# Performance work log

Hardware: AMD Instinct MI355X
Metric: run time of the kernel (lower is better)

## Reference

```python
import jax, jax.numpy as jnp
import numpy as np

N = 50000      # graph nodes
E = 400000     # random edges (plus N self-loops)
F = 128        # graph feature dim
H = 4          # GAT heads (layer1)
DH = 64        # gnn_hidden_size (per-head out, layer1)
EMB = 8        # emb_size / GAT final out
B = 16384      # batch
NS = 20        # number of sparse features
V = 1000       # vocab per sparse feature
DENSE = 64     # num_fea_size
HID = 256      # hidden_dims
EPS = 1e-5


def setup_inputs():
    key = jax.random.key(0)
    ks = jax.random.split(key, 40)
    loop = jnp.arange(N, dtype=jnp.int32)
    src = jnp.concatenate([jax.random.randint(ks[0], (E,), 0, N, dtype=jnp.int32), loop])
    dst = jnp.concatenate([jax.random.randint(ks[1], (E,), 0, N, dtype=jnp.int32), loop])
    s = 0.05
    d = {
        'X_id': jax.random.randint(ks[2], (B, 2), 0, N),
        'X_sparse': jax.random.randint(ks[3], (B, NS), 0, V),
        'X_dense': jax.random.normal(ks[4], (B, DENSE), jnp.float32),
        'emb_tables': jax.random.normal(ks[5], (NS, V, EMB), jnp.float32) * s,
        'graph_feature': jax.random.normal(ks[6], (N, F), jnp.float32),
        'src': src, 'dst': dst,
        'wide_w': jax.random.normal(ks[7], (EMB, DENSE), jnp.float32) * s,
        'wide_b': jnp.zeros((EMB,), jnp.float32),
        'lin1_w': jax.random.normal(ks[8], (HID, NS * EMB + DENSE), jnp.float32) * s,
        'lin1_b': jnp.zeros((HID,), jnp.float32),
        'bn1_g': jnp.ones((HID,), jnp.float32),
        'bn1_b': jnp.zeros((HID,), jnp.float32),
        'bn1_m': jax.random.normal(ks[9], (HID,), jnp.float32) * s,
        'bn1_v': jnp.ones((HID,), jnp.float32),
        'lin2_w': jax.random.normal(ks[10], (HID, HID), jnp.float32) * s,
        'lin2_b': jnp.zeros((HID,), jnp.float32),
        'bn2_g': jnp.ones((HID,), jnp.float32),
        'bn2_b': jnp.zeros((HID,), jnp.float32),
        'bn2_m': jax.random.normal(ks[11], (HID,), jnp.float32) * s,
        'bn2_v': jnp.ones((HID,), jnp.float32),
        'dnn_w': jax.random.normal(ks[12], (EMB, HID), jnp.float32) * s,
        'dnn_b': jnp.zeros((EMB,), jnp.float32),
        'gat1_w': jax.random.normal(ks[13], (H * DH, F), jnp.float32) * s,
        'gat1_al': jax.random.normal(ks[14], (H, DH), jnp.float32) * s,
        'gat1_ar': jax.random.normal(ks[15], (H, DH), jnp.float32) * s,
        'gat1_bias': jnp.zeros((H * DH,), jnp.float32),
        'gat2_w': jax.random.normal(ks[16], (EMB, H * DH), jnp.float32) * s,
        'gat2_al': jax.random.normal(ks[17], (1, EMB), jnp.float32) * s,
        'gat2_ar': jax.random.normal(ks[18], (1, EMB), jnp.float32) * s,
        'gat2_bias': jnp.zeros((EMB,), jnp.float32),
        'g1w': jax.random.normal(ks[19], (1, EMB), jnp.float32) * s,
        'g1b': jnp.zeros((1,), jnp.float32),
        'g2w': jax.random.normal(ks[20], (1, EMB), jnp.float32) * s,
        'g2b': jnp.zeros((1,), jnp.float32),
        'g3w': jax.random.normal(ks[21], (1, EMB), jnp.float32) * s,
        'g3b': jnp.zeros((1,), jnp.float32),
        'gout_w': jax.random.normal(ks[22], (2, 3 * EMB), jnp.float32) * s,
        'gout_b': jnp.zeros((2,), jnp.float32),
    }
    return d


def gat_conv(h, W, al, ar, bias, src, dst, heads, dh):
    # DGL GATConv: project, per-edge attention, edge-softmax over dst, aggregate
    feat = (h @ W.T).reshape(-1, heads, dh)          # [N, H, D]
    el = (feat * al).sum(-1)                          # [N, H] src score
    er = (feat * ar).sum(-1)                          # [N, H] dst score
    e = jax.nn.leaky_relu(el[src] + er[dst], 0.2)     # [Etot, H]
    emax = jax.lax.stop_gradient(jax.ops.segment_max(e, dst, num_segments=N))
    a = jnp.exp(e - emax[dst])
    denom = jax.ops.segment_sum(a, dst, num_segments=N)  # [N, H]
    alpha = a / denom[dst]                            # [Etot, H]
    out = jax.ops.segment_sum(alpha[:, :, None] * feat[src], dst, num_segments=N)
    return out + bias.reshape(1, heads, dh)           # [N, H, D]


def batchnorm_eval(x, g, b, m, v):
    return g * (x - m) * jax.lax.rsqrt(v + EPS) + b


def reference(X_id, X_sparse, X_dense, emb_tables, graph_feature, src, dst,
              wide_w, wide_b, lin1_w, lin1_b, bn1_g, bn1_b, bn1_m, bn1_v,
              lin2_w, lin2_b, bn2_g, bn2_b, bn2_m, bn2_v, dnn_w, dnn_b,
              gat1_w, gat1_al, gat1_ar, gat1_bias, gat2_w, gat2_al, gat2_ar, gat2_bias,
              g1w, g1b, g2w, g2b, g3w, g3b, gout_w, gout_b):
    commit_ids = X_id[:, 1]
    # sparse embedding lookup: [B, NS, EMB] -> [B, NS*EMB]
    sparse_embed = emb_tables[jnp.arange(NS)[None, :], X_sparse].reshape(B, NS * EMB)
    x = jnp.concatenate([sparse_embed, X_dense], axis=-1)
    wide_out = X_dense @ wide_w.T + wide_b            # [B, EMB]
    # deep MLP (eval-mode BN, dropout = identity)
    d = jax.nn.relu(batchnorm_eval(x @ lin1_w.T + lin1_b, bn1_g, bn1_b, bn1_m, bn1_v))
    d = jax.nn.relu(batchnorm_eval(d @ lin2_w.T + lin2_b, bn2_g, bn2_b, bn2_m, bn2_v))
    deep_out = d @ dnn_w.T + dnn_b                    # [B, EMB]
    # GAT
    h1 = gat_conv(graph_feature, gat1_w, gat1_al, gat1_ar, gat1_bias, src, dst, H, DH)
    h1 = jax.nn.elu(h1.reshape(N, H * DH))
    h2 = gat_conv(h1, gat2_w, gat2_al, gat2_ar, gat2_bias, src, dst, 1, EMB)
    gcn = h2.reshape(N, EMB)                          # squeeze head dim
    gcn_out = gcn[commit_ids]                         # [B, EMB]
    # Gate (concat)
    aw = jax.nn.sigmoid(wide_out @ g1w.T + g1b)
    bw = jax.nn.sigmoid(deep_out @ g2w.T + g2b)
    cw = jax.nn.sigmoid(gcn_out @ g3w.T + g3b)
    tot = aw + bw + cw
    combined = jnp.concatenate([(aw / tot) * wide_out, (bw / tot) * deep_out,
                                (cw / tot) * gcn_out], axis=1)
    out = combined @ gout_w.T + gout_b                # [B, 2]
    return jax.nn.softmax(out, axis=1)
```

## Files before the change

kernel.cpp:

```cpp
#include <hip/hip_runtime.h>

#define TPB 256
#define DCAP 64
constexpr float BN_EPS = 1e-5f;

typedef __attribute__((ext_vector_type(8))) short short8;
typedef __attribute__((ext_vector_type(4))) float floatx4;

__device__ __forceinline__ float sigmoidf_(float x) { return 1.f / (1.f + __expf(-x)); }
__device__ __forceinline__ unsigned short f2bf(float f) {
    unsigned u = __float_as_uint(f);
    u += 0x7FFFu + ((u >> 16) & 1u);
    return (unsigned short)(u >> 16);
}
__device__ __forceinline__ float bf2f(unsigned short h) {
    return __uint_as_float((unsigned)h << 16);
}

__global__ __launch_bounds__(TPB) void prep_kernel(
    const float* __restrict__ w1, unsigned short* __restrict__ o1,
    const float* __restrict__ w2, unsigned short* __restrict__ o2,
    const float* __restrict__ w3, unsigned short* __restrict__ o3,
    const float* __restrict__ gfeat, unsigned short* __restrict__ gfeatb, int ng4,
    const int* __restrict__ Xs, const float* __restrict__ Xd,
    const float* __restrict__ emb, unsigned short* __restrict__ x, int nx, int B)
{
    const int NW = 256 * 224 + 256 * 256 + 256 * 128;
    int idx = blockIdx.x * TPB + threadIdx.x;
    if (idx < NW) {
        if (idx < 256 * 224) o1[idx] = f2bf(w1[idx]);
        else if (idx < 256 * 224 + 256 * 256) o2[idx - 256 * 224] = f2bf(w2[idx - 256 * 224]);
        else o3[idx - 256 * 224 - 256 * 256] = f2bf(w3[idx - 256 * 224 - 256 * 256]);
        return;
    }
    int i = idx - NW;
    if (i < ng4) {
        float4 v = ((const float4*)gfeat)[i];
        ushort4 o;
        o.x = f2bf(v.x); o.y = f2bf(v.y); o.z = f2bf(v.z); o.w = f2bf(v.w);
        ((ushort4*)gfeatb)[i] = o;
        return;
    }
    i -= ng4;
    if (i >= nx) return;
    int b = i / 224, c = i - b * 224;
    float v;
    if (c < 160) {
        int s = c >> 3, j = c & 7;
        int e = Xs[b * 20 + s];
        v = emb[((size_t)s * 1000 + e) * 8 + j];
    } else {
        v = Xd[b * 64 + (c - 160)];
    }
    x[i] = f2bf(v);
}

template<bool BNRELU>
__global__ __launch_bounds__(256) void gemm_mfma(
    const unsigned short* __restrict__ A, const unsigned short* __restrict__ W,
    const float* __restrict__ bias,
    const float* __restrict__ g, const float* __restrict__ bb,
    const float* __restrict__ bm, const float* __restrict__ bv,
    unsigned short* __restrict__ C, int M, int N, int K)
{
    constexpr int SK = 40;
    __shared__ unsigned short As[64 * SK];
    __shared__ unsigned short Bs[64 * SK];
    int tid = threadIdx.x;
    int wave = tid >> 6, lane = tid & 63;
    int wm = (wave & 1) * 32, wn = (wave >> 1) * 32;
    int m0 = blockIdx.x * 64, n0 = blockIdx.y * 64;
    int lrow = lane & 15, lk = (lane >> 4) * 8;
    floatx4 acc[2][2] = {};
    for (int k0 = 0; k0 < K; k0 += 32) {
        {
            int r = tid >> 2, seg = (tid & 3) * 8;
            uint4 av = make_uint4(0u, 0u, 0u, 0u);
            int gm = m0 + r;
            if (gm < M) av = *(const uint4*)(A + (size_t)gm * K + k0 + seg);
            *(uint4*)(As + r * SK + seg) = av;
            uint4 wv = make_uint4(0u, 0u, 0u, 0u);
            int gn = n0 + r;
            if (gn < N) wv = *(const uint4*)(W + (size_t)gn * K + k0 + seg);
            *(uint4*)(Bs + r * SK + seg) = wv;
        }
        __syncthreads();
        short8 af[2], bfr[2];
#pragma unroll
        for (int i = 0; i < 2; ++i)
            af[i] = *(const short8*)(As + (wm + i * 16 + lrow) * SK + lk);
#pragma unroll
        for (int j = 0; j < 2; ++j)
            bfr[j] = *(const short8*)(Bs + (wn + j * 16 + lrow) * SK + lk);
#pragma unroll
        for (int i = 0; i < 2; ++i)
#pragma unroll
            for (int j = 0; j < 2; ++j)
                acc[i][j] = __builtin_amdgcn_mfma_f32_16x16x32_bf16(
                    af[i], bfr[j], acc[i][j], 0, 0, 0);
        __syncthreads();
    }
    int crow = (lane >> 4) * 4, ccol = lane & 15;
#pragma unroll
    for (int j = 0; j < 2; ++j) {
        int gn = n0 + wn + j * 16 + ccol;
        float sc = 1.f, sh = 0.f;
        if (BNRELU) {
            sc = g[gn] * rsqrtf(bv[gn] + BN_EPS);
            sh = (bias[gn] - bm[gn]) * sc + bb[gn];
        }
#pragma unroll
        for (int i = 0; i < 2; ++i) {
#pragma unroll
            for (int r = 0; r < 4; ++r) {
                int gm = m0 + wm + i * 16 + crow + r;
                if (gm >= M) continue;
                float t = acc[i][j][r];
                if (BNRELU) t = fmaxf(t * sc + sh, 0.f);
                C[(size_t)gm * N + gn] = f2bf(t);
            }
        }
    }
}

__global__ __launch_bounds__(TPB) void heads_kernel(
    const float* __restrict__ Xd, const float* __restrict__ Ww,
    const float* __restrict__ wb, float* __restrict__ wide,
    const unsigned short* __restrict__ d2, const float* __restrict__ Wd,
    const float* __restrict__ db, float* __restrict__ deep, int B)
{
    int nb = (B + 3) / 4;
    int lane = threadIdx.x & 63;
    float p[8];
    if ((int)blockIdx.x < nb) {
        int r = blockIdx.x * 4 + (threadIdx.x >> 6);
        if (r >= B) return;
        float a = Xd[(size_t)r * 64 + lane];
#pragma unroll
        for (int j = 0; j < 8; ++j) p[j] = a * Ww[j * 64 + lane];
#pragma unroll
        for (int off = 1; off < 64; off <<= 1)
#pragma unroll
            for (int j = 0; j < 8; ++j) p[j] += __shfl_xor(p[j], off, 64);
        if (lane == 0) {
#pragma unroll
            for (int j = 0; j < 8; ++j) wide[(size_t)r * 8 + j] = p[j] + wb[j];
        }
    } else {
        int r = (blockIdx.x - nb) * 4 + (threadIdx.x >> 6);
        if (r >= B) return;
        uint2 ab = *(const uint2*)(d2 + (size_t)r * 256 + lane * 4);
        float a0 = bf2f((unsigned short)(ab.x & 0xFFFFu));
        float a1 = bf2f((unsigned short)(ab.x >> 16));
        float a2 = bf2f((unsigned short)(ab.y & 0xFFFFu));
        float a3 = bf2f((unsigned short)(ab.y >> 16));
#pragma unroll
        for (int j = 0; j < 8; ++j) {
            float4 wv = *(const float4*)(Wd + j * 256 + lane * 4);
            p[j] = a0 * wv.x + a1 * wv.y + a2 * wv.z + a3 * wv.w;
        }
#pragma unroll
        for (int off = 1; off < 64; off <<= 1)
#pragma unroll
            for (int j = 0; j < 8; ++j) p[j] += __shfl_xor(p[j], off, 64);
        if (lane == 0) {
#pragma unroll
            for (int j = 0; j < 8; ++j) deep[(size_t)r * 8 + j] = p[j] + db[j];
        }
    }
}

template<int HN, int DHD>
__global__ __launch_bounds__(TPB) void attn_coef_bf16(
    const unsigned short* __restrict__ feat, const float* __restrict__ al,
    const float* __restrict__ ar, float* __restrict__ el, float* __restrict__ er, int Nn)
{
    int idx = blockIdx.x * TPB + threadIdx.x;
    if (idx >= Nn * HN) return;
    int n = idx / HN, h = idx - n * HN;
    const uint2* f4 = (const uint2*)(feat + (size_t)n * (HN * DHD) + h * DHD);
    const float4* al4 = (const float4*)(al + h * DHD);
    const float4* ar4 = (const float4*)(ar + h * DHD);
    float sl = 0.f, sr = 0.f;
#pragma unroll
    for (int d = 0; d < DHD / 4; ++d) {
        uint2 fb = f4[d];
        float f0 = bf2f((unsigned short)(fb.x & 0xFFFFu));
        float f1 = bf2f((unsigned short)(fb.x >> 16));
        float f2 = bf2f((unsigned short)(fb.y & 0xFFFFu));
        float f3 = bf2f((unsigned short)(fb.y >> 16));
        float4 lv = al4[d], rv = ar4[d];
        sl += f0 * lv.x + f1 * lv.y + f2 * lv.z + f3 * lv.w;
        sr += f0 * rv.x + f1 * rv.y + f2 * rv.z + f3 * rv.w;
    }
    el[idx] = sl; er[idx] = sr;
}

__global__ __launch_bounds__(TPB) void scatter_direct(
    const int* __restrict__ src, const int* __restrict__ dst,
    int* __restrict__ cnt, int* __restrict__ esrc, int E)
{
    int i = blockIdx.x * TPB + threadIdx.x;
    if (i >= E) return;
    int d = dst[i];
    int pos = atomicAdd(&cnt[d], 1);
    if (pos < DCAP) esrc[(size_t)d * DCAP + pos] = src[i];
}

__global__ __launch_bounds__(TPB) void gat1_gather_fused(
    const unsigned short* __restrict__ feat, const float* __restrict__ el,
    const float* __restrict__ er, const int* __restrict__ cnt,
    const int* __restrict__ esrc, const float* __restrict__ bias,
    const float* __restrict__ w2, const float* __restrict__ al2,
    const float* __restrict__ ar2,
    float* __restrict__ feat2, float* __restrict__ el2, float* __restrict__ er2, int Nn)
{
    int n = blockIdx.x * 4 + (threadIdx.x >> 6);
    if (n >= Nn) return;
    int lane = threadIdx.x & 63;
    int h = lane >> 4;
    int c = h * 64 + (lane & 15) * 4;
    float erv = er[n * 4 + h];
    int beg = n * DCAP;
    int deg = cnt[n]; if (deg > DCAP) deg = DCAP;
    int end = beg + deg;
    float4 acc = make_float4(0.f, 0.f, 0.f, 0.f);
    float dsum = 0.f;
    int e = beg;
    for (; e + 4 <= end; e += 4) {
        int sv[4]; float lv[4]; uint2 fb[4];
#pragma unroll
        for (int u = 0; u < 4; ++u) sv[u] = esrc[e + u];
#pragma unroll
        for (int u = 0; u < 4; ++u) lv[u] = el[sv[u] * 4 + h];
#pragma unroll
        for (int u = 0; u < 4; ++u) fb[u] = *(const uint2*)(feat + (size_t)sv[u] * 256 + c);
#pragma unroll
        for (int u = 0; u < 4; ++u) {
            float ev = lv[u] + erv;
            ev = ev > 0.f ? ev : 0.2f * ev;
            float av = __expf(ev);
            dsum += av;
            acc.x += av * bf2f((unsigned short)(fb[u].x & 0xFFFFu));
            acc.y += av * bf2f((unsigned short)(fb[u].x >> 16));
            acc.z += av * bf2f((unsigned short)(fb[u].y & 0xFFFFu));
            acc.w += av * bf2f((unsigned short)(fb[u].y >> 16));
        }
    }
    for (; e < end; ++e) {
        int s = esrc[e];
        float ev = el[s * 4 + h] + erv;
        ev = ev > 0.f ? ev : 0.2f * ev;
        float av = __expf(ev);
        dsum += av;
        uint2 fb = *(const uint2*)(feat + (size_t)s * 256 + c);
        acc.x += av * bf2f((unsigned short)(fb.x & 0xFFFFu));
        acc.y += av * bf2f((unsigned short)(fb.x >> 16));
        acc.z += av * bf2f((unsigned short)(fb.y & 0xFFFFu));
        acc.w += av * bf2f((unsigned short)(fb.y >> 16));
    }
    float inv = 1.f / dsum;
    float4 bv = *(const float4*)(bias + c);
    float4 o;
    o.x = acc.x * inv + bv.x; o.y = acc.y * inv + bv.y;
    o.z = acc.z * inv + bv.z; o.w = acc.w * inv + bv.w;
    o.x = o.x > 0.f ? o.x : __expf(o.x) - 1.f;
    o.y = o.y > 0.f ? o.y : __expf(o.y) - 1.f;
    o.z = o.z > 0.f ? o.z : __expf(o.z) - 1.f;
    o.w = o.w > 0.f ? o.w : __expf(o.w) - 1.f;
    float p[8];
#pragma unroll
    for (int j = 0; j < 8; ++j) {
        float4 wv = *(const float4*)(w2 + j * 256 + c);
        p[j] = o.x * wv.x + o.y * wv.y + o.z * wv.z + o.w * wv.w;
    }
#pragma unroll
    for (int off = 1; off < 64; off <<= 1)
#pragma unroll
        for (int j = 0; j < 8; ++j)
            p[j] += __shfl_xor(p[j], off, 64);
    if (lane == 0) {
        float e_l = 0.f, e_r = 0.f;
#pragma unroll
        for (int j = 0; j < 8; ++j) {
            feat2[(size_t)n * 8 + j] = p[j];
            e_l += p[j] * al2[j];
            e_r += p[j] * ar2[j];
        }
        el2[n] = e_l; er2[n] = e_r;
    }
}

__global__ __launch_bounds__(TPB) void gat2_final_kernel(
    const float* __restrict__ feat2, const float* __restrict__ el,
    const float* __restrict__ er, const int* __restrict__ cnt,
    const int* __restrict__ esrc, const int* __restrict__ Xid,
    const float* __restrict__ wide, const float* __restrict__ deep,
    const float* __restrict__ g2bias,
    const float* __restrict__ g1w, const float* __restrict__ g1b,
    const float* __restrict__ g2w, const float* __restrict__ g2b,
    const float* __restrict__ g3w, const float* __restrict__ g3b,
    const float* __restrict__ goutw, const float* __restrict__ goutb,
    float* __restrict__ out, int B)
{
    __shared__ float ls[256];
    int tid = threadIdx.x;
    int b = blockIdx.x * 32 + (tid >> 3), j = tid & 7;
    if (b < B) {
        int n = Xid[b * 2 + 1];
        float erv = er[n];
        int beg = n * DCAP;
        int deg = cnt[n]; if (deg > DCAP) deg = DCAP;
        int end = beg + deg;
        float acc = 0.f, dsum = 0.f;
        int e = beg;
        for (; e + 4 <= end; e += 4) {
            int sv[4]; float lv[4], fv[4];
#pragma unroll
            for (int u = 0; u < 4; ++u) sv[u] = esrc[e + u];
#pragma unroll
            for (int u = 0; u < 4; ++u) lv[u] = el[sv[u]];
#pragma unroll
            for (int u = 0; u < 4; ++u) fv[u] = feat2[(size_t)sv[u] * 8 + j];
#pragma unroll
            for (int u = 0; u < 4; ++u) {
                float ev = lv[u] + erv;
                ev = ev > 0.f ? ev : 0.2f * ev;
                float av = __expf(ev);
                dsum += av;
                acc += av * fv[u];
            }
        }
        for (; e < end; ++e) {
            int s = esrc[e];
            float ev = el[s] + erv;
            ev = ev > 0.f ? ev : 0.2f * ev;
            float av = __expf(ev);
            dsum += av;
            acc += av * feat2[(size_t)s * 8 + j];
        }
        ls[tid] = acc / dsum + g2bias[j];
    }
    __syncthreads();
    if (tid >= 32) return;
    int br = blockIdx.x * 32 + tid;
    if (br >= B) return;
    float w8[8], d8[8], g8[8];
    {
        float4 t0 = *(const float4*)(wide + (size_t)br * 8);
        float4 t1 = *(const float4*)(wide + (size_t)br * 8 + 4);
        w8[0] = t0.x; w8[1] = t0.y; w8[2] = t0.z; w8[3] = t0.w;
        w8[4] = t1.x; w8[5] = t1.y; w8[6] = t1.z; w8[7] = t1.w;
        t0 = *(const float4*)(deep + (size_t)br * 8);
        t1 = *(const float4*)(deep + (size_t)br * 8 + 4);
        d8[0] = t0.x; d8[1] = t0.y; d8[2] = t0.z; d8[3] = t0.w;
        d8[4] = t1.x; d8[5] = t1.y; d8[6] = t1.z; d8[7] = t1.w;
#pragma unroll
        for (int j2 = 0; j2 < 8; ++j2) g8[j2] = ls[tid * 8 + j2];
    }
    float s1 = g1b[0], s2 = g2b[0], s3 = g3b[0];
#pragma unroll
    for (int j2 = 0; j2 < 8; ++j2) { s1 += w8[j2] * g1w[j2]; s2 += d8[j2] * g2w[j2]; s3 += g8[j2] * g3w[j2]; }
    float aw = sigmoidf_(s1), bw = sigmoidf_(s2), cw = sigmoidf_(s3);
    float inv_tot = 1.f / (aw + bw + cw);
    float an = aw * inv_tot, bn = bw * inv_tot, cn = cw * inv_tot;
    float o0 = goutb[0], o1 = goutb[1];
#pragma unroll
    for (int j2 = 0; j2 < 8; ++j2) {
        float c0 = an * w8[j2]; o0 += goutw[j2] * c0;      o1 += goutw[24 + j2] * c0;
        float c1 = bn * d8[j2]; o0 += goutw[8 + j2] * c1;  o1 += goutw[32 + j2] * c1;
        float c2 = cn * g8[j2]; o0 += goutw[16 + j2] * c2; o1 += goutw[40 + j2] * c2;
    }
    float mx = fmaxf(o0, o1);
    float e0 = __expf(o0 - mx), e1 = __expf(o1 - mx);
    float inv = 1.f / (e0 + e1);
    out[(size_t)br * 2] = e0 * inv;
    out[(size_t)br * 2 + 1] = e1 * inv;
}

extern "C" void kernel_launch(void* const* d_in, const int* in_sizes, int n_in,
                              void* d_out, int out_size, void* d_ws, size_t ws_size,
                              hipStream_t stream)
{
    const int*   Xid    = (const int*)d_in[0];
    const int*   Xs     = (const int*)d_in[1];
    const float* Xd     = (const float*)d_in[2];
    const float* emb    = (const float*)d_in[3];
    const float* gfeat  = (const float*)d_in[4];
    const int*   src    = (const int*)d_in[5];
    const int*   dst    = (const int*)d_in[6];
    const float* wide_w = (const float*)d_in[7];
    const float* wide_b = (const float*)d_in[8];
    const float* lin1_w = (const float*)d_in[9];
    const float* lin1_b = (const float*)d_in[10];
    const float* bn1_g  = (const float*)d_in[11];
    const float* bn1_b  = (const float*)d_in[12];
    const float* bn1_m  = (const float*)d_in[13];
    const float* bn1_v  = (const float*)d_in[14];
    const float* lin2_w = (const float*)d_in[15];
    const float* lin2_b = (const float*)d_in[16];
    const float* bn2_g  = (const float*)d_in[17];
    const float* bn2_b  = (const float*)d_in[18];
    const float* bn2_m  = (const float*)d_in[19];
    const float* bn2_v  = (const float*)d_in[20];
    const float* dnn_w  = (const float*)d_in[21];
    const float* dnn_b  = (const float*)d_in[22];
    const float* gat1_w = (const float*)d_in[23];
    const float* gat1_al = (const float*)d_in[24];
    const float* gat1_ar = (const float*)d_in[25];
    const float* gat1_bias = (const float*)d_in[26];
    const float* gat2_w = (const float*)d_in[27];
    const float* gat2_al = (const float*)d_in[28];
    const float* gat2_ar = (const float*)d_in[29];
    const float* gat2_bias = (const float*)d_in[30];
    const float* g1w = (const float*)d_in[31];
    const float* g1b = (const float*)d_in[32];
    const float* g2w = (const float*)d_in[33];
    const float* g2b = (const float*)d_in[34];
    const float* g3w = (const float*)d_in[35];
    const float* g3b = (const float*)d_in[36];
    const float* goutw = (const float*)d_in[37];
    const float* goutb = (const float*)d_in[38];

    const int B    = in_sizes[0] / 2;
    const int Nn   = in_sizes[4] / 128;
    const int Etot = in_sizes[5];

    char* base = (char*)d_ws;
    size_t off = 0;
    auto alloc = [&](size_t bytes) -> char* {
        char* p = base + off;
        off += (bytes + 255) & ~(size_t)255;
        return p;
    };
    unsigned short* xb = (unsigned short*)alloc((size_t)B * 224 * 2);
    unsigned short* d1 = (unsigned short*)alloc((size_t)B * 256 * 2);
    unsigned short* d2 = (unsigned short*)alloc((size_t)B * 256 * 2);
    unsigned short* feat1  = (unsigned short*)alloc((size_t)Nn * 256 * 2);
    unsigned short* gfeatb = (unsigned short*)alloc((size_t)Nn * 128 * 2);
    unsigned short* w1b = (unsigned short*)alloc(256 * 224 * 2);
    unsigned short* w2b = (unsigned short*)alloc(256 * 256 * 2);
    unsigned short* wg1b = (unsigned short*)alloc(256 * 128 * 2);
    float* wide  = (float*)alloc((size_t)B * 8 * 4);
    float* deep  = (float*)alloc((size_t)B * 8 * 4);
    float* el1   = (float*)alloc((size_t)Nn * 4 * 4);
    float* er1   = (float*)alloc((size_t)Nn * 4 * 4);
    float* feat2 = (float*)alloc((size_t)Nn * 8 * 4);
    float* el2   = (float*)alloc((size_t)Nn * 4);
    float* er2   = (float*)alloc((size_t)Nn * 4);
    int* cnt     = (int*)alloc((size_t)Nn * 4);
    int* esrc    = (int*)alloc((size_t)Nn * DCAP * 4);

    hipMemsetAsync(cnt, 0, (size_t)Nn * sizeof(int), stream);
    scatter_direct<<<(Etot + TPB - 1) / TPB, TPB, 0, stream>>>(src, dst, cnt, esrc, Etot);

    {
        const int NW = 256 * 224 + 256 * 256 + 256 * 128;
        const int NG4 = Nn * 128 / 4;
        const int NX = B * 224;
        int total = NW + NG4 + NX;
        prep_kernel<<<(total + TPB - 1) / TPB, TPB, 0, stream>>>(
            lin1_w, w1b, lin2_w, w2b, gat1_w, wg1b,
            gfeat, gfeatb, NG4, Xs, Xd, emb, xb, NX, B);
    }

    gemm_mfma<true><<<dim3((B + 63) / 64, 4), 256, 0, stream>>>(
        xb, w1b, lin1_b, bn1_g, bn1_b, bn1_m, bn1_v, d1, B, 256, 224);
    gemm_mfma<true><<<dim3((B + 63) / 64, 4), 256, 0, stream>>>(
        d1, w2b, lin2_b, bn2_g, bn2_b, bn2_m, bn2_v, d2, B, 256, 256);
    heads_kernel<<<2 * ((B + 3) / 4), TPB, 0, stream>>>(
        Xd, wide_w, wide_b, wide, d2, dnn_w, dnn_b, deep, B);

    gemm_mfma<false><<<dim3((Nn + 63) / 64, 4), 256, 0, stream>>>(
        gfeatb, wg1b, nullptr, nullptr, nullptr, nullptr, nullptr, feat1, Nn, 256, 128);
    attn_coef_bf16<4, 64><<<(Nn * 4 + TPB - 1) / TPB, TPB, 0, stream>>>(
        feat1, gat1_al, gat1_ar, el1, er1, Nn);
    gat1_gather_fused<<<(Nn + 3) / 4, TPB, 0, stream>>>(
        feat1, el1, er1, cnt, esrc, gat1_bias,
        gat2_w, gat2_al, gat2_ar, feat2, el2, er2, Nn);

    gat2_final_kernel<<<(B + 31) / 32, TPB, 0, stream>>>(
        feat2, el2, er2, cnt, esrc, Xid, wide, deep, gat2_bias,
        g1w, g1b, g2w, g2b, g3w, g3b, goutw, goutb, (float*)d_out, B);
}
```

Baseline: 311.4 us.

## Merge independent DNN and GAT kernels into combined stage launches

Independent kernels from the DNN branch and the GAT branch are merged into four combined launches that split work by block index: scatter with prep, the lin1 GEMM with the GAT1 GEMM, the lin2 GEMM with the attention coefficients, and the heads with the GAT1 gather. This cuts the launch count and lets small kernels run alongside each other so the GPU stays filled. The cost is divergent block roles and shared-memory allocation in blocks that do not use it.

```diff
diff --git a/kernel.cpp b/kernel.cpp
--- a/kernel.cpp
+++ b/kernel.cpp
@@ -17,59 +17,20 @@
     return __uint_as_float((unsigned)h << 16);
 }
 
-__global__ __launch_bounds__(TPB) void prep_kernel(
-    const float* __restrict__ w1, unsigned short* __restrict__ o1,
-    const float* __restrict__ w2, unsigned short* __restrict__ o2,
-    const float* __restrict__ w3, unsigned short* __restrict__ o3,
-    const float* __restrict__ gfeat, unsigned short* __restrict__ gfeatb, int ng4,
-    const int* __restrict__ Xs, const float* __restrict__ Xd,
-    const float* __restrict__ emb, unsigned short* __restrict__ x, int nx, int B)
-{
-    const int NW = 256 * 224 + 256 * 256 + 256 * 128;
-    int idx = blockIdx.x * TPB + threadIdx.x;
-    if (idx < NW) {
-        if (idx < 256 * 224) o1[idx] = f2bf(w1[idx]);
-        else if (idx < 256 * 224 + 256 * 256) o2[idx - 256 * 224] = f2bf(w2[idx - 256 * 224]);
-        else o3[idx - 256 * 224 - 256 * 256] = f2bf(w3[idx - 256 * 224 - 256 * 256]);
-        return;
-    }
-    int i = idx - NW;
-    if (i < ng4) {
-        float4 v = ((const float4*)gfeat)[i];
-        ushort4 o;
-        o.x = f2bf(v.x); o.y = f2bf(v.y); o.z = f2bf(v.z); o.w = f2bf(v.w);
-        ((ushort4*)gfeatb)[i] = o;
-        return;
-    }
-    i -= ng4;
-    if (i >= nx) return;
-    int b = i / 224, c = i - b * 224;
-    float v;
-    if (c < 160) {
-        int s = c >> 3, j = c & 7;
-        int e = Xs[b * 20 + s];
-        v = emb[((size_t)s * 1000 + e) * 8 + j];
-    } else {
-        v = Xd[b * 64 + (c - 160)];
-    }
-    x[i] = f2bf(v);
-}
 
 template<bool BNRELU>
-__global__ __launch_bounds__(256) void gemm_mfma(
+__device__ __forceinline__ void gemm_dev(
     const unsigned short* __restrict__ A, const unsigned short* __restrict__ W,
     const float* __restrict__ bias,
     const float* __restrict__ g, const float* __restrict__ bb,
     const float* __restrict__ bm, const float* __restrict__ bv,
-    unsigned short* __restrict__ C, int M, int N, int K)
+    unsigned short* __restrict__ C, int M, int N, int K, int m0, int n0,
+    unsigned short* As, unsigned short* Bs)
 {
     constexpr int SK = 40;
-    __shared__ unsigned short As[64 * SK];
-    __shared__ unsigned short Bs[64 * SK];
     int tid = threadIdx.x;
     int wave = tid >> 6, lane = tid & 63;
     int wm = (wave & 1) * 32, wn = (wave >> 1) * 32;
-    int m0 = blockIdx.x * 64, n0 = blockIdx.y * 64;
     int lrow = lane & 15, lk = (lane >> 4) * 8;
     floatx4 acc[2][2] = {};
     for (int k0 = 0; k0 < K; k0 += 32) {
@@ -123,67 +84,108 @@
     }
 }
 
-__global__ __launch_bounds__(TPB) void heads_kernel(
-    const float* __restrict__ Xd, const float* __restrict__ Ww,
-    const float* __restrict__ wb, float* __restrict__ wide,
-    const unsigned short* __restrict__ d2, const float* __restrict__ Wd,
-    const float* __restrict__ db, float* __restrict__ deep, int B)
-{
-    int nb = (B + 3) / 4;
-    int lane = threadIdx.x & 63;
-    float p[8];
-    if ((int)blockIdx.x < nb) {
-        int r = blockIdx.x * 4 + (threadIdx.x >> 6);
-        if (r >= B) return;
-        float a = Xd[(size_t)r * 64 + lane];
-#pragma unroll
-        for (int j = 0; j < 8; ++j) p[j] = a * Ww[j * 64 + lane];
-#pragma unroll
-        for (int off = 1; off < 64; off <<= 1)
-#pragma unroll
-            for (int j = 0; j < 8; ++j) p[j] += __shfl_xor(p[j], off, 64);
-        if (lane == 0) {
-#pragma unroll
-            for (int j = 0; j < 8; ++j) wide[(size_t)r * 8 + j] = p[j] + wb[j];
-        }
+__global__ __launch_bounds__(TPB) void stageA_kernel(
+    const int* __restrict__ src, const int* __restrict__ dst,
+    int* __restrict__ cnt, int* __restrict__ esrc, int E, int sblk,
+    const float* __restrict__ w1, unsigned short* __restrict__ o1,
+    const float* __restrict__ w2, unsigned short* __restrict__ o2,
+    const float* __restrict__ w3, unsigned short* __restrict__ o3,
+    const float* __restrict__ gfeat, unsigned short* __restrict__ gfeatb, int ng4,
+    const int* __restrict__ Xs, const float* __restrict__ Xd,
+    const float* __restrict__ emb, unsigned short* __restrict__ x, int nx)
+{
+    if ((int)blockIdx.x < sblk) {
+        int i = blockIdx.x * TPB + threadIdx.x;
+        if (i >= E) return;
+        int d = dst[i];
+        int pos = atomicAdd(&cnt[d], 1);
+        if (pos < DCAP) esrc[(size_t)d * DCAP + pos] = src[i];
+        return;
+    }
+    const int NW = 256 * 224 + 256 * 256 + 256 * 128;
+    int idx = (blockIdx.x - sblk) * TPB + threadIdx.x;
+    if (idx < NW) {
+        if (idx < 256 * 224) o1[idx] = f2bf(w1[idx]);
+        else if (idx < 256 * 224 + 256 * 256) o2[idx - 256 * 224] = f2bf(w2[idx - 256 * 224]);
+        else o3[idx - 256 * 224 - 256 * 256] = f2bf(w3[idx - 256 * 224 - 256 * 256]);
+        return;
+    }
+    int i = idx - NW;
+    if (i < ng4) {
+        float4 v = ((const float4*)gfeat)[i];
+        ushort4 o;
+        o.x = f2bf(v.x); o.y = f2bf(v.y); o.z = f2bf(v.z); o.w = f2bf(v.w);
+        ((ushort4*)gfeatb)[i] = o;
+        return;
+    }
+    i -= ng4;
+    if (i >= nx) return;
+    int b = i / 224, c = i - b * 224;
+    float v;
+    if (c < 160) {
+        int s = c >> 3, j = c & 7;
+        int e = Xs[b * 20 + s];
+        v = emb[((size_t)s * 1000 + e) * 8 + j];
     } else {
-        int r = (blockIdx.x - nb) * 4 + (threadIdx.x >> 6);
-        if (r >= B) return;
-        uint2 ab = *(const uint2*)(d2 + (size_t)r * 256 + lane * 4);
-        float a0 = bf2f((unsigned short)(ab.x & 0xFFFFu));
-        float a1 = bf2f((unsigned short)(ab.x >> 16));
-        float a2 = bf2f((unsigned short)(ab.y & 0xFFFFu));
-        float a3 = bf2f((unsigned short)(ab.y >> 16));
-#pragma unroll
-        for (int j = 0; j < 8; ++j) {
-            float4 wv = *(const float4*)(Wd + j * 256 + lane * 4);
-            p[j] = a0 * wv.x + a1 * wv.y + a2 * wv.z + a3 * wv.w;
-        }
-#pragma unroll
-        for (int off = 1; off < 64; off <<= 1)
-#pragma unroll
-            for (int j = 0; j < 8; ++j) p[j] += __shfl_xor(p[j], off, 64);
-        if (lane == 0) {
-#pragma unroll
-            for (int j = 0; j < 8; ++j) deep[(size_t)r * 8 + j] = p[j] + db[j];
-        }
-    }
-}
-
-template<int HN, int DHD>
-__global__ __launch_bounds__(TPB) void attn_coef_bf16(
-    const unsigned short* __restrict__ feat, const float* __restrict__ al,
-    const float* __restrict__ ar, float* __restrict__ el, float* __restrict__ er, int Nn)
-{
-    int idx = blockIdx.x * TPB + threadIdx.x;
-    if (idx >= Nn * HN) return;
-    int n = idx / HN, h = idx - n * HN;
-    const uint2* f4 = (const uint2*)(feat + (size_t)n * (HN * DHD) + h * DHD);
-    const float4* al4 = (const float4*)(al + h * DHD);
-    const float4* ar4 = (const float4*)(ar + h * DHD);
+        v = Xd[b * 64 + (c - 160)];
+    }
+    x[i] = f2bf(v);
+}
+
+__global__ __launch_bounds__(256) void stageB_kernel(
+    const unsigned short* __restrict__ xb, const unsigned short* __restrict__ w1b,
+    const float* __restrict__ lin1_b,
+    const float* __restrict__ bn1_g, const float* __restrict__ bn1_b,
+    const float* __restrict__ bn1_m, const float* __restrict__ bn1_v,
+    unsigned short* __restrict__ d1, int B, int mb1,
+    const unsigned short* __restrict__ gfeatb, const unsigned short* __restrict__ wg1b,
+    unsigned short* __restrict__ feat1, int Nn, int mbf)
+{
+    __shared__ unsigned short As[64 * 40];
+    __shared__ unsigned short Bs[64 * 40];
+    int bid = blockIdx.x;
+    int nblk1 = mb1 * 4;
+    if (bid < nblk1) {
+        int bx = bid % mb1, by = bid / mb1;
+        gemm_dev<true>(xb, w1b, lin1_b, bn1_g, bn1_b, bn1_m, bn1_v,
+                       d1, B, 256, 224, bx * 64, by * 64, As, Bs);
+    } else {
+        int b2 = bid - nblk1;
+        int bx = b2 % mbf, by = b2 / mbf;
+        gemm_dev<false>(gfeatb, wg1b, nullptr, nullptr, nullptr, nullptr, nullptr,
+                        feat1, Nn, 256, 128, bx * 64, by * 64, As, Bs);
+    }
+}
+
+__global__ __launch_bounds__(256) void stageC_kernel(
+    const unsigned short* __restrict__ d1, const unsigned short* __restrict__ w2b,
+    const float* __restrict__ lin2_b,
+    const float* __restrict__ bn2_g, const float* __restrict__ bn2_b,
+    const float* __restrict__ bn2_m, const float* __restrict__ bn2_v,
+    unsigned short* __restrict__ d2, int B, int mb1,
+    const unsigned short* __restrict__ feat1,
+    const float* __restrict__ al, const float* __restrict__ ar,
+    float* __restrict__ el, float* __restrict__ er, int Nn)
+{
+    __shared__ unsigned short As[64 * 40];
+    __shared__ unsigned short Bs[64 * 40];
+    int bid = blockIdx.x;
+    int nblk2 = mb1 * 4;
+    if (bid < nblk2) {
+        int bx = bid % mb1, by = bid / mb1;
+        gemm_dev<true>(d1, w2b, lin2_b, bn2_g, bn2_b, bn2_m, bn2_v,
+                       d2, B, 256, 256, bx * 64, by * 64, As, Bs);
+        return;
+    }
+    int idx = (bid - nblk2) * TPB + threadIdx.x;
+    if (idx >= Nn * 4) return;
+    int n = idx >> 2, h = idx & 3;
+    const uint2* f4 = (const uint2*)(feat1 + (size_t)n * 256 + h * 64);
+    const float4* al4 = (const float4*)(al + h * 64);
+    const float4* ar4 = (const float4*)(ar + h * 64);
     float sl = 0.f, sr = 0.f;
 #pragma unroll
-    for (int d = 0; d < DHD / 4; ++d) {
+    for (int d = 0; d < 16; ++d) {
         uint2 fb = f4[d];
         float f0 = bf2f((unsigned short)(fb.x & 0xFFFFu));
         float f1 = bf2f((unsigned short)(fb.x >> 16));
@@ -196,28 +198,62 @@
     el[idx] = sl; er[idx] = sr;
 }
 
-__global__ __launch_bounds__(TPB) void scatter_direct(
-    const int* __restrict__ src, const int* __restrict__ dst,
-    int* __restrict__ cnt, int* __restrict__ esrc, int E)
-{
-    int i = blockIdx.x * TPB + threadIdx.x;
-    if (i >= E) return;
-    int d = dst[i];
-    int pos = atomicAdd(&cnt[d], 1);
-    if (pos < DCAP) esrc[(size_t)d * DCAP + pos] = src[i];
-}
-
-__global__ __launch_bounds__(TPB) void gat1_gather_fused(
+__global__ __launch_bounds__(TPB) void stageD_kernel(
+    const float* __restrict__ Xd, const float* __restrict__ Ww,
+    const float* __restrict__ wb, float* __restrict__ wide,
+    const unsigned short* __restrict__ d2, const float* __restrict__ Wd,
+    const float* __restrict__ db, float* __restrict__ deep, int B, int hblk,
     const unsigned short* __restrict__ feat, const float* __restrict__ el,
     const float* __restrict__ er, const int* __restrict__ cnt,
     const int* __restrict__ esrc, const float* __restrict__ bias,
-    const float* __restrict__ w2, const float* __restrict__ al2,
+    const float* __restrict__ w2g, const float* __restrict__ al2,
     const float* __restrict__ ar2,
     float* __restrict__ feat2, float* __restrict__ el2, float* __restrict__ er2, int Nn)
 {
-    int n = blockIdx.x * 4 + (threadIdx.x >> 6);
+    int lane = threadIdx.x & 63;
+    if ((int)blockIdx.x < hblk) {
+        int nb = (B + 3) / 4;
+        float p[8];
+        if ((int)blockIdx.x < nb) {
+            int r = blockIdx.x * 4 + (threadIdx.x >> 6);
+            if (r >= B) return;
+            float a = Xd[(size_t)r * 64 + lane];
+#pragma unroll
+            for (int j = 0; j < 8; ++j) p[j] = a * Ww[j * 64 + lane];
+#pragma unroll
+            for (int off = 1; off < 64; off <<= 1)
+#pragma unroll
+                for (int j = 0; j < 8; ++j) p[j] += __shfl_xor(p[j], off, 64);
+            if (lane == 0) {
+#pragma unroll
+                for (int j = 0; j < 8; ++j) wide[(size_t)r * 8 + j] = p[j] + wb[j];
+            }
+        } else {
+            int r = (blockIdx.x - nb) * 4 + (threadIdx.x >> 6);
+            if (r >= B) return;
+            uint2 ab = *(const uint2*)(d2 + (size_t)r * 256 + lane * 4);
+            float a0 = bf2f((unsigned short)(ab.x & 0xFFFFu));
+            float a1 = bf2f((unsigned short)(ab.x >> 16));
+            float a2 = bf2f((unsigned short)(ab.y & 0xFFFFu));
+            float a3 = bf2f((unsigned short)(ab.y >> 16));
+#pragma unroll
+            for (int j = 0; j < 8; ++j) {
+                float4 wv = *(const float4*)(Wd + j * 256 + lane * 4);
+                p[j] = a0 * wv.x + a1 * wv.y + a2 * wv.z + a3 * wv.w;
+            }
+#pragma unroll
+            for (int off = 1; off < 64; off <<= 1)
+#pragma unroll
+                for (int j = 0; j < 8; ++j) p[j] += __shfl_xor(p[j], off, 64);
+            if (lane == 0) {
+#pragma unroll
+                for (int j = 0; j < 8; ++j) deep[(size_t)r * 8 + j] = p[j] + db[j];
+            }
+        }
+        return;
+    }
+    int n = (blockIdx.x - hblk) * 4 + (threadIdx.x >> 6);
     if (n >= Nn) return;
-    int lane = threadIdx.x & 63;
     int h = lane >> 4;
     int c = h * 64 + (lane & 15) * 4;
     float erv = er[n * 4 + h];
@@ -271,7 +307,7 @@
     float p[8];
 #pragma unroll
     for (int j = 0; j < 8; ++j) {
-        float4 wv = *(const float4*)(w2 + j * 256 + c);
+        float4 wv = *(const float4*)(w2g + j * 256 + c);
         p[j] = o.x * wv.x + o.y * wv.y + o.z * wv.z + o.w * wv.w;
     }
 #pragma unroll
@@ -452,32 +488,41 @@
     int* esrc    = (int*)alloc((size_t)Nn * DCAP * 4);
 
     hipMemsetAsync(cnt, 0, (size_t)Nn * sizeof(int), stream);
-    scatter_direct<<<(Etot + TPB - 1) / TPB, TPB, 0, stream>>>(src, dst, cnt, esrc, Etot);
 
     {
+        const int sblk = (Etot + TPB - 1) / TPB;
         const int NW = 256 * 224 + 256 * 256 + 256 * 128;
         const int NG4 = Nn * 128 / 4;
         const int NX = B * 224;
-        int total = NW + NG4 + NX;
-        prep_kernel<<<(total + TPB - 1) / TPB, TPB, 0, stream>>>(
+        const int pblk = (NW + NG4 + NX + TPB - 1) / TPB;
+        stageA_kernel<<<sblk + pblk, TPB, 0, stream>>>(
+            src, dst, cnt, esrc, Etot, sblk,
             lin1_w, w1b, lin2_w, w2b, gat1_w, wg1b,
-            gfeat, gfeatb, NG4, Xs, Xd, emb, xb, NX, B);
-    }
-
-    gemm_mfma<true><<<dim3((B + 63) / 64, 4), 256, 0, stream>>>(
-        xb, w1b, lin1_b, bn1_g, bn1_b, bn1_m, bn1_v, d1, B, 256, 224);
-    gemm_mfma<true><<<dim3((B + 63) / 64, 4), 256, 0, stream>>>(
-        d1, w2b, lin2_b, bn2_g, bn2_b, bn2_m, bn2_v, d2, B, 256, 256);
-    heads_kernel<<<2 * ((B + 3) / 4), TPB, 0, stream>>>(
-        Xd, wide_w, wide_b, wide, d2, dnn_w, dnn_b, deep, B);
-
-    gemm_mfma<false><<<dim3((Nn + 63) / 64, 4), 256, 0, stream>>>(
-        gfeatb, wg1b, nullptr, nullptr, nullptr, nullptr, nullptr, feat1, Nn, 256, 128);
-    attn_coef_bf16<4, 64><<<(Nn * 4 + TPB - 1) / TPB, TPB, 0, stream>>>(
-        feat1, gat1_al, gat1_ar, el1, er1, Nn);
-    gat1_gather_fused<<<(Nn + 3) / 4, TPB, 0, stream>>>(
-        feat1, el1, er1, cnt, esrc, gat1_bias,
-        gat2_w, gat2_al, gat2_ar, feat2, el2, er2, Nn);
+            gfeat, gfeatb, NG4, Xs, Xd, emb, xb, NX);
+    }
+
+    const int mb1 = (B + 63) / 64;
+    const int mbf = (Nn + 63) / 64;
+
+    stageB_kernel<<<mb1 * 4 + mbf * 4, 256, 0, stream>>>(
+        xb, w1b, lin1_b, bn1_g, bn1_b, bn1_m, bn1_v, d1, B, mb1,
+        gfeatb, wg1b, feat1, Nn, mbf);
+
+    {
+        const int ablk = (Nn * 4 + TPB - 1) / TPB;
+        stageC_kernel<<<mb1 * 4 + ablk, 256, 0, stream>>>(
+            d1, w2b, lin2_b, bn2_g, bn2_b, bn2_m, bn2_v, d2, B, mb1,
+            feat1, gat1_al, gat1_ar, el1, er1, Nn);
+    }
+
+    {
+        const int hblk = 2 * ((B + 3) / 4);
+        const int gblk = (Nn + 3) / 4;
+        stageD_kernel<<<hblk + gblk, TPB, 0, stream>>>(
+            Xd, wide_w, wide_b, wide, d2, dnn_w, dnn_b, deep, B, hblk,
+            feat1, el1, er1, cnt, esrc, gat1_bias,
+            gat2_w, gat2_al, gat2_ar, feat2, el2, er2, Nn);
+    }
 
     gat2_final_kernel<<<(B + 31) / 32, TPB, 0, stream>>>(
         feat2, el2, er2, cnt, esrc, Xid, wide, deep, gat2_bias,
```

Result: faster. 291.4 us (-6.4%).
